# Kernel optimization log

Hardware: AMD Instinct MI355X
Metric: run time of the kernel (lower is better)

## Reference

```python
import jax, jax.numpy as jnp
import numpy as np

EMB = 1024
NH = 16
DH = EMB // NH
SCALE = np.sqrt(EMB).astype(np.float32)  # module scales by sqrt(emb_dim), not sqrt(d_head)


def setup_inputs() -> dict:
    key = jax.random.key(0)
    ks = jax.random.split(key, 9)
    s = 1.0 / np.sqrt(EMB)
    return {
        "a": jax.random.normal(ks[0], (4, 2048, EMB), jnp.float32),
        "Wq": jax.random.normal(ks[1], (EMB, EMB), jnp.float32) * s,
        "bq": jnp.zeros((EMB,), jnp.float32),
        "Wk": jax.random.normal(ks[2], (EMB, EMB), jnp.float32) * s,
        "bk": jnp.zeros((EMB,), jnp.float32),
        "Wv": jax.random.normal(ks[3], (EMB, EMB), jnp.float32) * s,
        "bv": jnp.zeros((EMB,), jnp.float32),
        "Wo": jax.random.normal(ks[4], (EMB, EMB), jnp.float32) * s,
        "bo": jnp.zeros((EMB,), jnp.float32),
    }


def reference(a, Wq, bq, Wk, bk, Wv, bv, Wo, bo):
    N, S, _ = a.shape
    # Q/K/V projections (self-attention: b is None -> b = a)
    Q = (a @ Wq + bq).reshape(N, S, NH, DH).transpose(0, 2, 1, 3)  # [N,H,A,D]
    K = (a @ Wk + bk).reshape(N, S, NH, DH).transpose(0, 2, 1, 3)  # [N,H,B,D]
    V = (a @ Wv + bv).reshape(N, S, NH, DH).transpose(0, 2, 1, 3)  # [N,H,B,D]
    score = jnp.einsum('nhad,nhbd->nhab', Q, K) / SCALE
    score = jax.nn.softmax(score, axis=-1)
    out = jnp.einsum('nhab,nhbd->nhad', score, V)                  # [N,H,A,D]
    out = out.transpose(0, 2, 1, 3).reshape(N, S, EMB)
    return out @ Wo + bo
```

## Files before the change

### kernel.cpp

```cpp
#include <hip/hip_runtime.h>
#include <hip/hip_bf16.h>
#include <stdint.h>

typedef __attribute__((ext_vector_type(8))) short short8v;
typedef __attribute__((ext_vector_type(4))) float float4v;

#define GLDS16(gp, lp) __builtin_amdgcn_global_load_lds( \
    (const __attribute__((address_space(1))) void*)(gp),  \
    (__attribute__((address_space(3))) void*)(lp), 16, 0, 0)

#if __has_builtin(__builtin_amdgcn_exp2f)
#define EXP2(x) __builtin_amdgcn_exp2f(x)
#else
#define EXP2(x) exp2f(x)
#endif

#define LOG2E 1.4426950408889634f

__global__ __launch_bounds__(256) void cast_a_kernel(
    const float* __restrict__ src, __hip_bfloat16* __restrict__ dst, int n4) {
  int i = blockIdx.x * blockDim.x + threadIdx.x;
  if (i < n4) {
    float4 v = ((const float4*)src)[i];
    union { __hip_bfloat16 h[4]; ushort4 u; } p;
    p.h[0] = __float2bfloat16(v.x);
    p.h[1] = __float2bfloat16(v.y);
    p.h[2] = __float2bfloat16(v.z);
    p.h[3] = __float2bfloat16(v.w);
    ((ushort4*)dst)[i] = p.u;
  }
}

__global__ __launch_bounds__(256) void transpose4_kernel(
    const float* __restrict__ Wq, const float* __restrict__ Wk,
    const float* __restrict__ Wv, const float* __restrict__ Wo,
    __hip_bfloat16* __restrict__ Wcat, __hip_bfloat16* __restrict__ WoT) {
  __shared__ float t[32][33];
  const int z = blockIdx.z;
  const float* W = (z == 0) ? Wq : (z == 1) ? Wk : (z == 2) ? Wv : Wo;
  __hip_bfloat16* dst = (z < 3) ? (Wcat + (size_t)z * 1048576) : WoT;
  int tx = threadIdx.x & 31, ty = threadIdx.x >> 5;
  int r0 = blockIdx.y * 32, c0 = blockIdx.x * 32;
#pragma unroll
  for (int i = 0; i < 4; ++i) {
    int r = ty + i * 8;
    t[r][tx] = W[(size_t)(r0 + r) * 1024 + c0 + tx];
  }
  __syncthreads();
#pragma unroll
  for (int i = 0; i < 4; ++i) {
    int r = ty + i * 8;
    dst[(size_t)(c0 + r) * 1024 + r0 + tx] = __float2bfloat16(t[tx][r]);
  }
}

__global__ __launch_bounds__(512, 2) void gemm_qkv8_kernel(
    const __hip_bfloat16* __restrict__ A, const __hip_bfloat16* __restrict__ BT,
    const float* __restrict__ bq, const float* __restrict__ bk,
    const float* __restrict__ bv, __hip_bfloat16* __restrict__ Qh,
    __hip_bfloat16* __restrict__ Kh, __hip_bfloat16* __restrict__ Vt) {
  __shared__ char lds[131072];
  const int tid = threadIdx.x;
  const int l = tid & 63, w = tid >> 6;
  const int g = l >> 4, cc = l & 15;
  const int wm = w >> 2, wn = w & 3;
  const int sw = (cc & 7) << 4;
  const int bid = blockIdx.x;
  const int nbid = (bid & 7) * 48 + (bid >> 3);
  const int tm = nbid / 12, tn = nbid % 12;
  const int m0 = tm * 256, n0 = tn * 256;

  const int scol = ((tid & 7) * 16) ^ (((tid >> 3) & 7) << 4);
  const char* pA = (const char*)A + (size_t)(m0 + (tid >> 3)) * 2048 + scol;
  const char* pB = (const char*)BT + (size_t)(n0 + (tid >> 3)) * 2048 + scol;
  char* ldsT = lds + tid * 16;

#define STGH(pG, base, half, kt) {                                            \
    GLDS16((pG) + ((half) * 128) * 2048 + (kt) * 128,                         \
           ldsT + (base) + (half) * 16384);                                   \
    GLDS16((pG) + ((half) * 128 + 64) * 2048 + (kt) * 128,                    \
           ldsT + (base) + (half) * 16384 + 8192);                            \
  }

  short8v af[4][2], bf[4][2];
#define DSA(base, fmb)                                                        \
  _Pragma("unroll") for (int i = 0; i < 4; ++i)                               \
  _Pragma("unroll") for (int kk = 0; kk < 2; ++kk)                            \
    af[i][kk] = *(const short8v*)(lds + (base) +                              \
        (((wm * 128 + ((fmb) + i) * 16 + cc) * 128 + kk * 64 + g * 16) ^ sw));
#define DSB(base, np)                                                        \
  _Pragma("unroll") for (int ii = 0; ii < 2; ++ii)                            \
  _Pragma("unroll") for (int kk = 0; kk < 2; ++kk)                            \
    bf[(np) * 2 + ii][kk] = *(const short8v*)(lds + (base) +                  \
        (((wn * 64 + ((np) * 2 + ii) * 16 + cc) * 128 + kk * 64 + g * 16) ^ sw));

  float4v acc[8][4];
#pragma unroll
  for (int m = 0; m < 8; ++m)
#pragma unroll
    for (int n = 0; n < 4; ++n) acc[m][n] = (float4v){0.f, 0.f, 0.f, 0.f};

#define MM(fmb, np)                                                           \
  __builtin_amdgcn_s_setprio(1);                                              \
  _Pragma("unroll") for (int i = 0; i < 4; ++i)                               \
  _Pragma("unroll") for (int ii = 0; ii < 2; ++ii)                            \
  _Pragma("unroll") for (int kk = 0; kk < 2; ++kk)                            \
    acc[(fmb) + i][(np) * 2 + ii] = __builtin_amdgcn_mfma_f32_16x16x32_bf16(  \
        af[i][kk], bf[(np) * 2 + ii][kk], acc[(fmb) + i][(np) * 2 + ii], 0, 0, 0); \
  __builtin_amdgcn_s_setprio(0);

#define BAR() __builtin_amdgcn_s_barrier()
#define WAIT4() asm volatile("s_waitcnt vmcnt(4)" ::: "memory")

  STGH(pB, 65536, 0, 0); STGH(pB, 65536, 1, 0);
  STGH(pA, 0, 0, 0);     STGH(pA, 0, 1, 0);
  STGH(pB, 98304, 0, 1); STGH(pB, 98304, 1, 1);
  WAIT4();
  BAR();

  for (int j = 0; j < 8; ++j) {
    const int vv = 2 * j + 1;
    const int u2 = (j < 7) ? 2 * j + 2 : 15;
    const int v2 = (j < 7) ? 2 * j + 3 : 15;
    DSA(0, 0); DSB(65536, 0);
    STGH(pA, 32768, 0, vv);
    BAR(); MM(0, 0); BAR();
    DSB(65536, 1);
    STGH(pA, 32768, 1, vv);
    BAR(); MM(0, 1); BAR();
    DSA(0, 4);
    STGH(pB, 65536, 0, u2);
    BAR(); MM(4, 0); BAR();
    STGH(pB, 65536, 1, u2);
    WAIT4();
    BAR(); MM(4, 1); BAR();
    DSA(32768, 0); DSB(98304, 0);
    STGH(pA, 0, 0, u2);
    BAR(); MM(0, 0); BAR();
    DSB(98304, 1);
    STGH(pA, 0, 1, u2);
    BAR(); MM(0, 1); BAR();
    DSA(32768, 4);
    STGH(pB, 98304, 0, v2);
    BAR(); MM(4, 0); BAR();
    STGH(pB, 98304, 1, v2);
    WAIT4();
    BAR(); MM(4, 1); BAR();
  }
#undef STGH
#undef DSA
#undef DSB
#undef MM
#undef BAR
#undef WAIT4

  const int sec = n0 >> 10;
  if (sec < 2) {
    __hip_bfloat16* out = sec == 0 ? Qh : Kh;
    const float* bias = sec == 0 ? bq : bk;
    const float scale = sec == 0 ? (LOG2E / 32.f) : 1.f;
#pragma unroll
    for (int m = 0; m < 8; ++m) {
#pragma unroll
      for (int n = 0; n < 4; ++n) {
        int colc = (n0 + wn * 64 + n * 16 + cc) & 1023;
        float b = bias[colc];
        int h = colc >> 6, d = colc & 63;
#pragma unroll
        for (int r = 0; r < 4; ++r) {
          int grow = m0 + wm * 128 + m * 16 + g * 4 + r;
          int nb = grow >> 11, s = grow & 2047;
          out[((size_t)(nb * 16 + h) * 2048 + s) * 64 + d] =
              __float2bfloat16((acc[m][n][r] + b) * scale);
        }
      }
    }
  } else {
#pragma unroll
    for (int m = 0; m < 8; ++m) {
      int grow0 = m0 + wm * 128 + m * 16 + g * 4;
      int nb = grow0 >> 11, key0 = grow0 & 2047;
      int kp0 = (key0 & ~31) | ((key0 & 12) << 1) | (((key0 >> 4) & 1) << 2);
#pragma unroll
      for (int n = 0; n < 4; ++n) {
        int colc = (n0 + wn * 64 + n * 16 + cc) & 1023;
        float b = bv[colc];
        int h = colc >> 6, d = colc & 63;
        union { __hip_bfloat16 h4[4]; uint2 u; } pk;
#pragma unroll
        for (int r = 0; r < 4; ++r) pk.h4[r] = __float2bfloat16(acc[m][n][r] + b);
        *(uint2*)&Vt[((size_t)((nb * 16 + h) * 64 + d)) * 2048 + kp0] = pk.u;
      }
    }
  }
}

__global__ __launch_bounds__(256, 2) void gemm_o_kernel(
    const __hip_bfloat16* __restrict__ A, const __hip_bfloat16* __restrict__ BT,
    const float* __restrict__ bias, float* __restrict__ C) {
  __shared__ char lds[32768];
  const int tid = threadIdx.x;
  const int l = tid & 63, w = tid >> 6;
  const int g = l >> 4, cc = l & 15;
  const int bid = blockIdx.x;
  const int nbid = (bid & 7) * 64 + (bid >> 3);
  const int m0 = (nbid & 63) * 128, n0 = (nbid >> 6) * 128;
  const int wm = w >> 1, wn = w & 1;

  float4v acc[4][4];
#pragma unroll
  for (int m = 0; m < 4; ++m)
#pragma unroll
    for (int n = 0; n < 4; ++n) acc[m][n] = (float4v){0.f, 0.f, 0.f, 0.f};

  for (int kt = 0; kt < 16; ++kt) {
#pragma unroll
    for (int j = 0; j < 4; ++j) {
      int ci = (w * 4 + j) * 64 + l;
      int row = ci >> 3, ko = (ci & 7) * 16;
      GLDS16((const char*)A + (size_t)(m0 + row) * 2048 + kt * 128 + ko,
             lds + ci * 16);
      GLDS16((const char*)BT + (size_t)(n0 + row) * 2048 + kt * 128 + ko,
             lds + 16384 + ci * 16);
    }
    __syncthreads();
#pragma unroll
    for (int h = 0; h < 2; ++h) {
      short8v af[4], bf[4];
#pragma unroll
      for (int m = 0; m < 4; ++m)
        af[m] = *(const short8v*)(lds + (wm * 64 + m * 16 + cc) * 128 + h * 64 + g * 16);
#pragma unroll
      for (int n = 0; n < 4; ++n)
        bf[n] = *(const short8v*)(lds + 16384 + (wn * 64 + n * 16 + cc) * 128 + h * 64 + g * 16);
#pragma unroll
      for (int m = 0; m < 4; ++m)
#pragma unroll
        for (int n = 0; n < 4; ++n)
          acc[m][n] = __builtin_amdgcn_mfma_f32_16x16x32_bf16(af[m], bf[n], acc[m][n], 0, 0, 0);
    }
    __syncthreads();
  }

#pragma unroll
  for (int m = 0; m < 4; ++m) {
    int row = m0 + wm * 64 + m * 16 + g * 4;
#pragma unroll
    for (int n = 0; n < 4; ++n) {
      int col = n0 + wn * 64 + n * 16 + cc;
      float b = bias[col];
#pragma unroll
      for (int r = 0; r < 4; ++r)
        C[(size_t)(row + r) * 1024 + col] = acc[m][n][r] + b;
    }
  }
}

__global__ __launch_bounds__(512, 4) void attn_kernel(
    const __hip_bfloat16* __restrict__ Q,
    const __hip_bfloat16* __restrict__ K,
    const __hip_bfloat16* __restrict__ VT,
    __hip_bfloat16* __restrict__ AO) {
  __shared__ char sK[4][8192];
  __shared__ char sV[4][8192];
  const int tid = threadIdx.x;
  const int l = tid & 63, w = tid >> 6;
  const int g = l >> 4, cc = l & 15;
  const int bid = blockIdx.x;
  const int nbid = (bid & 7) * 64 + (bid >> 3);
  const int bx = nbid & 7, nh = nbid >> 3;
  const int q0 = bx * 256 + w * 32;
  const char* Kb = (const char*)(K + (size_t)nh * 131072);
  const char* Vb = (const char*)(VT + (size_t)nh * 131072);
  const __hip_bfloat16* Qb = Q + (size_t)nh * 131072;

  short8v qf[2][2];
#pragma unroll
  for (int qg = 0; qg < 2; ++qg)
#pragma unroll
    for (int dh = 0; dh < 2; ++dh)
      qf[qg][dh] = *(const short8v*)(Qb + (size_t)(q0 + qg * 16 + cc) * 64 + dh * 32 + g * 8);

  int koff[4][2], voff[4][2];
#pragma unroll
  for (int kg = 0; kg < 4; ++kg)
#pragma unroll
    for (int dh = 0; dh < 2; ++dh) {
      int row = kg * 16 + cc;
      koff[kg][dh] = (row * 128 + dh * 64 + g * 16) ^ ((row & 7) << 4);
    }
#pragma unroll
  for (int f = 0; f < 4; ++f)
#pragma unroll
    for (int hh = 0; hh < 2; ++hh) {
      int d = f * 16 + cc;
      voff[f][hh] = (d * 128 + hh * 64 + g * 16) ^ ((d & 7) << 4);
    }
  const int ss = tid * 16;
  const int sr = ss >> 7;
  const int soff = (ss & 127) ^ ((sr & 7) << 4);
  const int stKo = sr * 128 + soff;
  const int stVo = sr * 4096 + soff;

  const short8v fone = {16256, 16256, 16256, 16256, 16256, 16256, 16256, 16256};

  float lr[2] = {0.f, 0.f};
  float4v oacc[2][4];
#pragma unroll
  for (int qg = 0; qg < 2; ++qg)
#pragma unroll
    for (int f = 0; f < 4; ++f) oacc[qg][f] = (float4v){0.f, 0.f, 0.f, 0.f};

#define STAGE(kb, vb, ktv)                                                    \
  {                                                                           \
    GLDS16(Kb + (size_t)(ktv) * 8192 + stKo, (kb) + ss);                      \
    GLDS16(Vb + (size_t)(ktv) * 128 + stVo, (vb) + ss);                       \
  }

#define TILE(KSRC, VSRC)                                                      \
  {                                                                           \
    short8v kf[4][2];                                                         \
    _Pragma("unroll") for (int kg = 0; kg < 4; ++kg)                          \
    _Pragma("unroll") for (int dh = 0; dh < 2; ++dh)                          \
      kf[kg][dh] = *(const short8v*)((KSRC) + koff[kg][dh]);                  \
    short8v pf[2][2];                                                         \
    _Pragma("unroll") for (int qg = 0; qg < 2; ++qg) {                        \
      float4v sv[4];                                                          \
      _Pragma("unroll") for (int kg = 0; kg < 4; ++kg) {                      \
        float4v z = (float4v){0.f, 0.f, 0.f, 0.f};                            \
        z = __builtin_amdgcn_mfma_f32_16x16x32_bf16(kf[kg][0], qf[qg][0], z, 0, 0, 0); \
        sv[kg] = __builtin_amdgcn_mfma_f32_16x16x32_bf16(kf[kg][1], qf[qg][1], z, 0, 0, 0); \
      }                                                                       \
      _Pragma("unroll") for (int kg = 0; kg < 4; ++kg)                        \
      _Pragma("unroll") for (int r = 0; r < 4; ++r) sv[kg][r] = EXP2(sv[kg][r]); \
      _Pragma("unroll") for (int hh = 0; hh < 2; ++hh) {                      \
        union { __hip_bfloat16 h[8]; short8v v8; } pk;                        \
        _Pragma("unroll") for (int jj = 0; jj < 4; ++jj) {                    \
          pk.h[jj]     = __float2bfloat16(sv[2 * hh][jj]);                    \
          pk.h[4 + jj] = __float2bfloat16(sv[2 * hh + 1][jj]);                \
        }                                                                     \
        pf[qg][hh] = pk.v8;                                                   \
      }                                                                       \
      float4v t = (float4v){0.f, 0.f, 0.f, 0.f};                              \
      t = __builtin_amdgcn_mfma_f32_16x16x32_bf16(fone, pf[qg][0], t, 0, 0, 0); \
      t = __builtin_amdgcn_mfma_f32_16x16x32_bf16(fone, pf[qg][1], t, 0, 0, 0); \
      lr[qg] += t[0];                                                         \
    }                                                                         \
    _Pragma("unroll") for (int f = 0; f < 4; ++f)                             \
    _Pragma("unroll") for (int hh = 0; hh < 2; ++hh) {                        \
      short8v vk = *(const short8v*)((VSRC) + voff[f][hh]);                   \
      _Pragma("unroll") for (int qg = 0; qg < 2; ++qg)                        \
        oacc[qg][f] = __builtin_amdgcn_mfma_f32_16x16x32_bf16(vk, pf[qg][hh], oacc[qg][f], 0, 0, 0); \
    }                                                                         \
  }

  STAGE(sK[0], sV[0], 0);
  STAGE(sK[1], sV[1], 1);

#pragma unroll 1
  for (int j = 0; j < 16; ++j) {
    asm volatile("s_waitcnt vmcnt(0)" ::: "memory");
    __builtin_amdgcn_s_barrier();
    const int p = (j & 1) << 1;
    const int s = p ^ 2;
    if (j < 15) {
      STAGE(sK[s], sV[s], 2 * j + 2);
      STAGE(sK[s + 1], sV[s + 1], 2 * j + 3);
    }
    TILE(sK[p], sV[p]);
    TILE(sK[p + 1], sV[p + 1]);
  }
#undef STAGE
#undef TILE

  int nb = nh >> 4, h = nh & 15;
#pragma unroll
  for (int qg = 0; qg < 2; ++qg) {
    float inv = 1.f / lr[qg];
    int qrow = q0 + qg * 16 + cc;
#pragma unroll
    for (int f = 0; f < 4; ++f)
#pragma unroll
      for (int r = 0; r < 4; ++r) {
        int d = f * 16 + g * 4 + r;
        AO[(size_t)(nb * 2048 + qrow) * 1024 + h * 64 + d] =
            __float2bfloat16(oacc[qg][f][r] * inv);
      }
  }
}

extern "C" void kernel_launch(void* const* d_in, const int* in_sizes, int n_in,
                              void* d_out, int out_size, void* d_ws, size_t ws_size,
                              hipStream_t stream) {
  const float* a  = (const float*)d_in[0];
  const float* Wq = (const float*)d_in[1];
  const float* bq = (const float*)d_in[2];
  const float* Wk = (const float*)d_in[3];
  const float* bk = (const float*)d_in[4];
  const float* Wv = (const float*)d_in[5];
  const float* bv = (const float*)d_in[6];
  const float* Wo = (const float*)d_in[7];
  const float* bo = (const float*)d_in[8];

  char* ws = (char*)d_ws;
  __hip_bfloat16* aB   = (__hip_bfloat16*)(ws);
  __hip_bfloat16* Wcat = (__hip_bfloat16*)(ws + (16ull << 20));
  __hip_bfloat16* WoT  = (__hip_bfloat16*)(ws + (22ull << 20));
  __hip_bfloat16* Qh   = (__hip_bfloat16*)(ws + (24ull << 20));
  __hip_bfloat16* Kh   = (__hip_bfloat16*)(ws + (40ull << 20));
  __hip_bfloat16* Vt   = (__hip_bfloat16*)(ws + (56ull << 20));
  __hip_bfloat16* AOb  = (__hip_bfloat16*)(ws + (72ull << 20));

  cast_a_kernel<<<8192, 256, 0, stream>>>(a, aB, 8192 * 1024 / 4);
  dim3 tg(32, 32, 4);
  transpose4_kernel<<<tg, 256, 0, stream>>>(Wq, Wk, Wv, Wo, Wcat, WoT);

  gemm_qkv8_kernel<<<384, 512, 0, stream>>>(aB, Wcat, bq, bk, bv, Qh, Kh, Vt);

  attn_kernel<<<512, 512, 0, stream>>>(Qh, Kh, Vt, AOb);

  gemm_o_kernel<<<512, 256, 0, stream>>>(AOb, WoT, bo, (float*)d_out);
}
```

Measured before the change: 178.6 us.

## Retile QKV GEMM to 256x192 tiles with 512 blocks and new pipeline

Changes the fused QKV projection GEMM from 256x256 tiles (384 blocks) to 256x192 tiles (512 blocks), so the grid splits evenly across the 256 compute units in two waves instead of leaving a partial wave. The wave layout becomes 4x2 with 64x96 per wave, the LDS staging and double-buffer schedule are rewritten with full vmcnt waits, and launch bounds drop to one block per CU. Because tiles can now straddle the Q/K/V boundary, the epilogue picks the output section per 16-column fragment. Smaller tiles lower arithmetic intensity and the stricter waits may expose more load latency.

```diff
diff --git a/kernel.cpp b/kernel.cpp
--- a/kernel.cpp
+++ b/kernel.cpp
@@ -54,138 +54,125 @@
   }
 }
 
-__global__ __launch_bounds__(512, 2) void gemm_qkv8_kernel(
+__global__ __launch_bounds__(512, 1) void gemm_qkv8_kernel(
     const __hip_bfloat16* __restrict__ A, const __hip_bfloat16* __restrict__ BT,
     const float* __restrict__ bq, const float* __restrict__ bk,
     const float* __restrict__ bv, __hip_bfloat16* __restrict__ Qh,
     __hip_bfloat16* __restrict__ Kh, __hip_bfloat16* __restrict__ Vt) {
-  __shared__ char lds[131072];
+  __shared__ char lds[114688];
   const int tid = threadIdx.x;
   const int l = tid & 63, w = tid >> 6;
   const int g = l >> 4, cc = l & 15;
-  const int wm = w >> 2, wn = w & 3;
+  const int wm = w >> 1, wn = w & 1;
   const int sw = (cc & 7) << 4;
   const int bid = blockIdx.x;
-  const int nbid = (bid & 7) * 48 + (bid >> 3);
-  const int tm = nbid / 12, tn = nbid % 12;
-  const int m0 = tm * 256, n0 = tn * 256;
+  const int nbid = (bid & 7) * 64 + (bid >> 3);
+  const int tm = nbid >> 4, tn = nbid & 15;
+  const int m0 = tm * 256, n0 = tn * 192;
 
   const int scol = ((tid & 7) * 16) ^ (((tid >> 3) & 7) << 4);
   const char* pA = (const char*)A + (size_t)(m0 + (tid >> 3)) * 2048 + scol;
   const char* pB = (const char*)BT + (size_t)(n0 + (tid >> 3)) * 2048 + scol;
   char* ldsT = lds + tid * 16;
 
-#define STGH(pG, base, half, kt) {                                            \
-    GLDS16((pG) + ((half) * 128) * 2048 + (kt) * 128,                         \
-           ldsT + (base) + (half) * 16384);                                   \
-    GLDS16((pG) + ((half) * 128 + 64) * 2048 + (kt) * 128,                    \
-           ldsT + (base) + (half) * 16384 + 8192);                            \
-  }
-
-  short8v af[4][2], bf[4][2];
-#define DSA(base, fmb)                                                        \
+#define STGA4(base, kt) {                                                     \
+    _Pragma("unroll") for (int L = 0; L < 4; ++L)                             \
+      GLDS16(pA + (size_t)L * 131072 + (kt) * 128, ldsT + (base) + L * 8192); \
+  }
+#define STGB3(base, kt) {                                                     \
+    _Pragma("unroll") for (int T = 0; T < 3; ++T)                             \
+      GLDS16(pB + (size_t)T * 131072 + (kt) * 128, ldsT + (base) + T * 8192); \
+  }
+
+  short8v af[4][2], bf[2][2];
+#define DSA(base)                                                             \
   _Pragma("unroll") for (int i = 0; i < 4; ++i)                               \
   _Pragma("unroll") for (int kk = 0; kk < 2; ++kk)                            \
     af[i][kk] = *(const short8v*)(lds + (base) +                              \
-        (((wm * 128 + ((fmb) + i) * 16 + cc) * 128 + kk * 64 + g * 16) ^ sw));
-#define DSB(base, np)                                                        \
+        (((wm * 64 + i * 16 + cc) * 128 + kk * 64 + g * 16) ^ sw));
+#define DSB(base, np)                                                         \
   _Pragma("unroll") for (int ii = 0; ii < 2; ++ii)                            \
   _Pragma("unroll") for (int kk = 0; kk < 2; ++kk)                            \
-    bf[(np) * 2 + ii][kk] = *(const short8v*)(lds + (base) +                  \
-        (((wn * 64 + ((np) * 2 + ii) * 16 + cc) * 128 + kk * 64 + g * 16) ^ sw));
-
-  float4v acc[8][4];
-#pragma unroll
-  for (int m = 0; m < 8; ++m)
-#pragma unroll
-    for (int n = 0; n < 4; ++n) acc[m][n] = (float4v){0.f, 0.f, 0.f, 0.f};
-
-#define MM(fmb, np)                                                           \
+    bf[ii][kk] = *(const short8v*)(lds + (base) +                             \
+        (((wn * 96 + (np) * 32 + ii * 16 + cc) * 128 + kk * 64 + g * 16) ^ sw));
+
+  float4v acc[4][6];
+#pragma unroll
+  for (int m = 0; m < 4; ++m)
+#pragma unroll
+    for (int n = 0; n < 6; ++n) acc[m][n] = (float4v){0.f, 0.f, 0.f, 0.f};
+
+#define MM(np)                                                                \
   __builtin_amdgcn_s_setprio(1);                                              \
   _Pragma("unroll") for (int i = 0; i < 4; ++i)                               \
   _Pragma("unroll") for (int ii = 0; ii < 2; ++ii)                            \
   _Pragma("unroll") for (int kk = 0; kk < 2; ++kk)                            \
-    acc[(fmb) + i][(np) * 2 + ii] = __builtin_amdgcn_mfma_f32_16x16x32_bf16(  \
-        af[i][kk], bf[(np) * 2 + ii][kk], acc[(fmb) + i][(np) * 2 + ii], 0, 0, 0); \
+    acc[i][(np) * 2 + ii] = __builtin_amdgcn_mfma_f32_16x16x32_bf16(          \
+        af[i][kk], bf[ii][kk], acc[i][(np) * 2 + ii], 0, 0, 0);               \
   __builtin_amdgcn_s_setprio(0);
 
 #define BAR() __builtin_amdgcn_s_barrier()
-#define WAIT4() asm volatile("s_waitcnt vmcnt(4)" ::: "memory")
-
-  STGH(pB, 65536, 0, 0); STGH(pB, 65536, 1, 0);
-  STGH(pA, 0, 0, 0);     STGH(pA, 0, 1, 0);
-  STGH(pB, 98304, 0, 1); STGH(pB, 98304, 1, 1);
-  WAIT4();
+
+  STGA4(0, 0);
+  STGB3(65536, 0);
+  asm volatile("s_waitcnt vmcnt(0)" ::: "memory");
   BAR();
 
   for (int j = 0; j < 8; ++j) {
     const int vv = 2 * j + 1;
     const int u2 = (j < 7) ? 2 * j + 2 : 15;
-    const int v2 = (j < 7) ? 2 * j + 3 : 15;
-    DSA(0, 0); DSB(65536, 0);
-    STGH(pA, 32768, 0, vv);
-    BAR(); MM(0, 0); BAR();
+    DSA(0); DSB(65536, 0);
+    STGA4(32768, vv);
+    BAR(); MM(0); BAR();
     DSB(65536, 1);
-    STGH(pA, 32768, 1, vv);
-    BAR(); MM(0, 1); BAR();
-    DSA(0, 4);
-    STGH(pB, 65536, 0, u2);
-    BAR(); MM(4, 0); BAR();
-    STGH(pB, 65536, 1, u2);
-    WAIT4();
-    BAR(); MM(4, 1); BAR();
-    DSA(32768, 0); DSB(98304, 0);
-    STGH(pA, 0, 0, u2);
-    BAR(); MM(0, 0); BAR();
-    DSB(98304, 1);
-    STGH(pA, 0, 1, u2);
-    BAR(); MM(0, 1); BAR();
-    DSA(32768, 4);
-    STGH(pB, 98304, 0, v2);
-    BAR(); MM(4, 0); BAR();
-    STGH(pB, 98304, 1, v2);
-    WAIT4();
-    BAR(); MM(4, 1); BAR();
-  }
-#undef STGH
+    STGB3(90112, vv);
+    BAR(); MM(1); BAR();
+    DSB(65536, 2);
+    STGA4(0, u2);
+    BAR(); MM(2); BAR();
+    asm volatile("s_waitcnt vmcnt(4)" ::: "memory");
+    BAR();
+    DSA(32768); DSB(90112, 0);
+    STGB3(65536, u2);
+    BAR(); MM(0); BAR();
+    DSB(90112, 1);
+    BAR(); MM(1); BAR();
+    DSB(90112, 2);
+    BAR(); MM(2); BAR();
+    asm volatile("s_waitcnt vmcnt(0)" ::: "memory");
+    BAR();
+  }
+#undef STGA4
+#undef STGB3
 #undef DSA
 #undef DSB
 #undef MM
 #undef BAR
-#undef WAIT4
-
-  const int sec = n0 >> 10;
-  if (sec < 2) {
-    __hip_bfloat16* out = sec == 0 ? Qh : Kh;
-    const float* bias = sec == 0 ? bq : bk;
-    const float scale = sec == 0 ? (LOG2E / 32.f) : 1.f;
-#pragma unroll
-    for (int m = 0; m < 8; ++m) {
-#pragma unroll
-      for (int n = 0; n < 4; ++n) {
-        int colc = (n0 + wn * 64 + n * 16 + cc) & 1023;
-        float b = bias[colc];
-        int h = colc >> 6, d = colc & 63;
+
+#pragma unroll
+  for (int m = 0; m < 4; ++m) {
+    int grow0 = m0 + wm * 64 + m * 16 + g * 4;
+    int nb = grow0 >> 11, key0 = grow0 & 2047;
+    int kp0 = (key0 & ~31) | ((key0 & 12) << 1) | (((key0 >> 4) & 1) << 2);
+#pragma unroll
+    for (int n = 0; n < 6; ++n) {
+      int col0 = n0 + wn * 96 + n * 16;
+      int sec = col0 >> 10;
+      int colc = (col0 & 1023) + cc;
+      int h = colc >> 6, d = colc & 63;
+      if (sec < 2) {
+        __hip_bfloat16* out = sec == 0 ? Qh : Kh;
+        float b = (sec == 0 ? bq : bk)[colc];
+        float scale = sec == 0 ? (LOG2E / 32.f) : 1.f;
 #pragma unroll
         for (int r = 0; r < 4; ++r) {
-          int grow = m0 + wm * 128 + m * 16 + g * 4 + r;
-          int nb = grow >> 11, s = grow & 2047;
+          int grow = grow0 + r;
+          int s = grow & 2047;
           out[((size_t)(nb * 16 + h) * 2048 + s) * 64 + d] =
               __float2bfloat16((acc[m][n][r] + b) * scale);
         }
-      }
-    }
-  } else {
-#pragma unroll
-    for (int m = 0; m < 8; ++m) {
-      int grow0 = m0 + wm * 128 + m * 16 + g * 4;
-      int nb = grow0 >> 11, key0 = grow0 & 2047;
-      int kp0 = (key0 & ~31) | ((key0 & 12) << 1) | (((key0 >> 4) & 1) << 2);
-#pragma unroll
-      for (int n = 0; n < 4; ++n) {
-        int colc = (n0 + wn * 64 + n * 16 + cc) & 1023;
+      } else {
         float b = bv[colc];
-        int h = colc >> 6, d = colc & 63;
         union { __hip_bfloat16 h4[4]; uint2 u; } pk;
 #pragma unroll
         for (int r = 0; r < 4; ++r) pk.h4[r] = __float2bfloat16(acc[m][n][r] + b);
@@ -415,7 +402,7 @@
   dim3 tg(32, 32, 4);
   transpose4_kernel<<<tg, 256, 0, stream>>>(Wq, Wk, Wv, Wo, Wcat, WoT);
 
-  gemm_qkv8_kernel<<<384, 512, 0, stream>>>(aB, Wcat, bq, bk, bv, Qh, Kh, Vt);
+  gemm_qkv8_kernel<<<512, 512, 0, stream>>>(aB, Wcat, bq, bk, bv, Qh, Kh, Vt);
 
   attn_kernel<<<512, 512, 0, stream>>>(Qh, Kh, Vt, AOb);
 
```

Measured after the change: 184.4 us. +3.2%, slower.
